# Optimization experiments

Measured on AMD Instinct MI355X. Metric: run time of the kernel, lower is better.

Reference implementation:

```python
import jax, jax.numpy as jnp
import numpy as np
import math

DIM = 512
HEADS = 8
DIM_HEAD = 64
INNER = HEADS * DIM_HEAD
B = 2
N = 2048


def _alibi_slopes(heads):
    def pow2(n):
        start = 2 ** (-2 ** (-(math.log2(n) - 3)))
        return [start * start ** i for i in range(n)]
    if math.log2(heads).is_integer():
        return pow2(heads)
    cp2 = 2 ** math.floor(math.log2(heads))
    return pow2(cp2) + pow2(2 * cp2)[0::2][: heads - cp2]


def setup_inputs() -> dict:
    key = jax.random.key(0)
    ks = jax.random.split(key, 9)
    s = 0.02
    return {
        "x": jax.random.normal(ks[0], (B, N, DIM), dtype=jnp.float32),
        "gamma": jnp.ones((DIM,), jnp.float32),
        "beta": jnp.zeros((DIM,), jnp.float32),
        "wq1": jax.random.normal(ks[1], (INNER, DIM), jnp.float32) * s,
        "wqd": jax.random.normal(ks[2], (INNER, 3), jnp.float32) * s,
        "wk1": jax.random.normal(ks[3], (INNER, DIM), jnp.float32) * s,
        "wkd": jax.random.normal(ks[4], (INNER, 3), jnp.float32) * s,
        "wv1": jax.random.normal(ks[5], (INNER, DIM), jnp.float32) * s,
        "wvd": jax.random.normal(ks[6], (INNER, 3), jnp.float32) * s,
        "wout": jax.random.normal(ks[7], (DIM, INNER), jnp.float32) * s,
    }


def _proj(xp, w1, wd):
    # xp: [b, dim, n+2] (already left-padded by 2)
    y = jnp.einsum('ed,bdn->ben', w1, xp)  # pointwise conv (kernel 1, no bias)
    # depthwise causal conv, kernel 3: valid conv after left pad of 2
    y = (wd[None, :, 0:1] * y[..., :-2]
         + wd[None, :, 1:2] * y[..., 1:-1]
         + wd[None, :, 2:3] * y[..., 2:])
    return y  # [b, inner, n]


def _split_heads(y, b, n):
    # [b, (h d), n] -> [b, h, n, d]
    return y.reshape(b, HEADS, DIM_HEAD, n).transpose(0, 1, 3, 2)


def reference(x, gamma, beta, wq1, wqd, wk1, wkd, wv1, wvd, wout):
    b, n, d = x.shape
    scale = DIM_HEAD ** -0.5
    # LayerNorm over last dim
    mu = jnp.mean(x, axis=-1, keepdims=True)
    var = jnp.var(x, axis=-1, keepdims=True)
    xn = (x - mu) / jnp.sqrt(var + 1e-5) * gamma + beta
    # b n d -> b d n, left pad 2
    xp = jnp.pad(xn.transpose(0, 2, 1), ((0, 0), (0, 0), (2, 0)))
    q = _split_heads(_proj(xp, wq1, wqd), b, n) * scale
    k = _split_heads(_proj(xp, wk1, wkd), b, n)
    v = _split_heads(_proj(xp, wv1, wvd), b, n)
    sim = jnp.einsum('bhid,bhjd->bhij', q, k)
    # ALiBi bias
    slopes = jnp.asarray(_alibi_slopes(HEADS), dtype=sim.dtype)  # [h]
    idx = jnp.arange(n)
    bias = -jnp.abs(idx[None, :] - idx[:, None]).astype(sim.dtype)  # [n, n]
    sim = sim + bias[None, None] * slopes[None, :, None, None]
    # causal mask
    causal = jnp.triu(jnp.ones((n, n), bool), 1)
    sim = jnp.where(causal[None, None], -jnp.finfo(sim.dtype).max, sim)
    attn = jax.nn.softmax(sim, axis=-1)
    out = jnp.einsum('bhij,bhjd->bhid', attn, v)
    out = out.transpose(0, 2, 1, 3).reshape(b, n, INNER)
    return out @ wout.T
```

## Files before the change

### kernel.cpp

```cpp
#include <hip/hip_runtime.h>
#include <hip/hip_bf16.h>
#include <math.h>

#define BATCH 2
#define NSEQ 2048
#define DIM 512
#define HEADS 8
#define DH 64
#define NTOK (BATCH * NSEQ)
#define NPROJ (3 * DIM)

typedef short short8 __attribute__((ext_vector_type(8)));
typedef short short4v __attribute__((ext_vector_type(4)));
typedef float f32x4 __attribute__((ext_vector_type(4)));
typedef float f32x16 __attribute__((ext_vector_type(16)));
typedef __hip_bfloat16 bf16;

static __device__ __forceinline__ short f2b(float f) {
    __hip_bfloat16 h = __float2bfloat16(f);
    return *(short*)&h;
}

static __device__ __forceinline__ void gload_lds16(const void* g, void* l) {
    __builtin_amdgcn_global_load_lds(
        (const __attribute__((address_space(1))) unsigned int*)g,
        (__attribute__((address_space(3))) unsigned int*)l, 16, 0, 0);
}

__global__ __launch_bounds__(128) void ln_kernel(
    const float* __restrict__ x, const float* __restrict__ gamma,
    const float* __restrict__ beta, bf16* __restrict__ xnb)
{
    int row = blockIdx.x;
    int tid = threadIdx.x;
    float4 v = ((const float4*)(x + (size_t)row * DIM))[tid];
    float s  = v.x + v.y + v.z + v.w;
    float s2 = v.x*v.x + v.y*v.y + v.z*v.z + v.w*v.w;
    #pragma unroll
    for (int off = 32; off > 0; off >>= 1) {
        s  += __shfl_down(s,  off);
        s2 += __shfl_down(s2, off);
    }
    __shared__ float red[4];
    if ((tid & 63) == 0) { red[(tid >> 6) * 2] = s; red[(tid >> 6) * 2 + 1] = s2; }
    __syncthreads();
    float S  = red[0] + red[2];
    float S2 = red[1] + red[3];
    float mu  = S * (1.0f / DIM);
    float var = S2 * (1.0f / DIM) - mu * mu;
    float inv = rsqrtf(var + 1e-5f);
    float4 g  = ((const float4*)gamma)[tid];
    float4 be = ((const float4*)beta)[tid];
    short4v o;
    o[0] = f2b((v.x - mu) * inv * g.x + be.x);
    o[1] = f2b((v.y - mu) * inv * g.y + be.y);
    o[2] = f2b((v.z - mu) * inv * g.z + be.z);
    o[3] = f2b((v.w - mu) * inv * g.w + be.w);
    ((short4v*)(xnb + (size_t)row * DIM))[tid] = o;
}

__global__ __launch_bounds__(256) void convert_w(
    const float* __restrict__ wq1, const float* __restrict__ wk1,
    const float* __restrict__ wv1, const float* __restrict__ wout,
    bf16* __restrict__ Wcat, bf16* __restrict__ woutb)
{
    int i4 = blockIdx.x * 256 + threadIdx.x;
    int base = i4 * 4;
    int which = base >> 18;
    int e = base & 262143;
    const float* src = which == 0 ? wq1 : which == 1 ? wk1 : which == 2 ? wv1 : wout;
    float4 v = *(const float4*)(src + e);
    bf16* dst = (which < 3) ? (Wcat + ((size_t)which << 18) + e) : (woutb + e);
    short4v o;
    o[0] = f2b(v.x); o[1] = f2b(v.y); o[2] = f2b(v.z); o[3] = f2b(v.w);
    *(short4v*)dst = o;
}

__global__ __launch_bounds__(256) void gemm_bf16_nt(
    const bf16* __restrict__ A, const bf16* __restrict__ W,
    float* __restrict__ C, int N, int K)
{
    __shared__ bf16 As[128 * 64];
    __shared__ bf16 Bs[128 * 64];
    int tid = threadIdx.x;
    int m0 = blockIdx.y * 128, n0 = blockIdx.x * 128;
    int lane = tid & 63;
    int w = tid >> 6;
    int wm = (w >> 1) * 64, wn = (w & 1) * 64;
    int l15 = lane & 15, l4 = lane >> 4;
    f32x4 acc[4][4] = {};
    for (int k0 = 0; k0 < K; k0 += 64) {
        __syncthreads();
        #pragma unroll
        for (int it = 0; it < 4; it++) {
            int s = it * 256 + tid;
            int row = s >> 3, cs = s & 7;
            gload_lds16(A + (size_t)(m0 + row) * K + k0 + cs * 8, As + s * 8);
            gload_lds16(W + (size_t)(n0 + row) * K + k0 + cs * 8, Bs + s * 8);
        }
        __syncthreads();
        #pragma unroll
        for (int kk = 0; kk < 64; kk += 32) {
            short8 af[4], bfr[4];
            #pragma unroll
            for (int m = 0; m < 4; m++)
                af[m] = *(const short8*)(As + (wm + m * 16 + l15) * 64 + kk + l4 * 8);
            #pragma unroll
            for (int n = 0; n < 4; n++)
                bfr[n] = *(const short8*)(Bs + (wn + n * 16 + l15) * 64 + kk + l4 * 8);
            #pragma unroll
            for (int m = 0; m < 4; m++)
                #pragma unroll
                for (int n = 0; n < 4; n++)
                    acc[m][n] = __builtin_amdgcn_mfma_f32_16x16x32_bf16(
                        af[m], bfr[n], acc[m][n], 0, 0, 0);
        }
    }
    #pragma unroll
    for (int m = 0; m < 4; m++)
        #pragma unroll
        for (int n = 0; n < 4; n++) {
            int row = m0 + wm + m * 16 + l4 * 4;
            int col = n0 + wn + n * 16 + l15;
            #pragma unroll
            for (int r = 0; r < 4; r++)
                C[(size_t)(row + r) * N + col] = acc[m][n][r];
        }
}

__global__ __launch_bounds__(256) void dwconv_kernel(
    const float* __restrict__ ycat,
    const float* __restrict__ wqd, const float* __restrict__ wkd, const float* __restrict__ wvd,
    bf16* __restrict__ q, bf16* __restrict__ k, bf16* __restrict__ v)
{
    int which = blockIdx.z;
    const float* wd = which == 0 ? wqd : which == 1 ? wkd : wvd;
    bf16* dst       = which == 0 ? q   : which == 1 ? k   : v;
    float scale     = which == 0 ? 0.125f : 1.0f;
    int idx = blockIdx.x * 256 + threadIdx.x;
    int e = idx & (DIM - 1);
    int t = idx >> 9;
    int n = t & (NSEQ - 1);
    const float* y = ycat + which * DIM;
    float y0 = y[(size_t)t * NPROJ + e];
    float y1 = (n >= 1) ? y[(size_t)(t - 1) * NPROJ + e] : 0.0f;
    float y2 = (n >= 2) ? y[(size_t)(t - 2) * NPROJ + e] : 0.0f;
    float w0 = wd[e * 3 + 0], w1 = wd[e * 3 + 1], w2 = wd[e * 3 + 2];
    float r = (w0 * y2 + w1 * y1 + w2 * y0) * scale;
    int b = t >> 11;
    int h = e >> 6, d = e & 63;
    dst[(((size_t)(b * HEADS + h)) * NSEQ + n) * DH + d] = __float2bfloat16(r);
}

__global__ __launch_bounds__(256) void vtrans_kernel(
    const bf16* __restrict__ v, bf16* __restrict__ vT)
{
    __shared__ unsigned short L[64][72];
    int bh = blockIdx.y;
    int n0 = blockIdx.x * 64;
    int tid = threadIdx.x;
    const unsigned short* src = (const unsigned short*)v + ((size_t)bh * NSEQ + n0) * DH;
    #pragma unroll
    for (int it = 0; it < 2; it++) {
        int idx = it * 256 + tid;
        int r = idx >> 3, c = (idx & 7) * 8;
        *(short8*)&L[r][c] = *(const short8*)(src + (size_t)r * DH + c);
    }
    __syncthreads();
    unsigned short* dst = (unsigned short*)vT + (size_t)bh * DH * NSEQ + n0;
    #pragma unroll
    for (int it = 0; it < 2; it++) {
        int idx = it * 256 + tid;
        int d = idx >> 3, c8 = (idx & 7) * 8;
        short8 o;
        #pragma unroll
        for (int t = 0; t < 8; t++) o[t] = (short)L[c8 + t][d];
        *(short8*)(dst + (size_t)d * NSEQ + c8) = o;
    }
}

struct KV { short8 kf[4]; short8 v0[2]; short8 v1[2]; };

__device__ __forceinline__ KV load_kv(
    const bf16* __restrict__ Kb, const unsigned short* __restrict__ vt,
    int j0, int il, int hi)
{
    KV r;
    const short8* krow = (const short8*)(Kb + (size_t)(j0 + il) * DH);
    #pragma unroll
    for (int c = 0; c < 4; c++) r.kf[c] = krow[2 * c + hi];
    #pragma unroll
    for (int jc = 0; jc < 2; jc++) {
        r.v0[jc] = *(const short8*)(vt + (size_t)il * NSEQ + j0 + jc * 16 + hi * 8);
        r.v1[jc] = *(const short8*)(vt + (size_t)(32 + il) * NSEQ + j0 + jc * 16 + hi * 8);
    }
    return r;
}

template<bool MASKED>
__device__ __forceinline__ void attn_step(
    const KV& kv, int j0, int il, int hi, int i_global,
    const short8* qf, const float* bconst, float slope2,
    f32x16& o0, f32x16& o1, float& lsum)
{
    f32x16 st = {};
    #pragma unroll
    for (int c = 0; c < 4; c++)
        st = __builtin_amdgcn_mfma_f32_32x32x16_bf16(kv.kf[c], qf[c], st, 0, 0, 0);
    float sdb = slope2 * (float)(j0 - i_global);
    float p[16];
    #pragma unroll
    for (int r = 0; r < 16; r++) {
        float e = fmaf(st[r], 1.4426950408889634f, sdb + bconst[r]);
        float pr = exp2f(e);
        if (MASKED) {
            int jl = (r & 3) + 8 * (r >> 2) + 4 * hi;
            pr = (jl <= il) ? pr : 0.0f;
        }
        p[r] = pr;
        lsum += pr;
    }
    unsigned w[8];
    #pragma unroll
    for (int g = 0; g < 4; g++) {
        asm("v_cvt_pk_bf16_f32 %0, %1, %2" : "=v"(w[2*g])   : "v"(p[4*g]),   "v"(p[4*g+1]));
        asm("v_cvt_pk_bf16_f32 %0, %1, %2" : "=v"(w[2*g+1]) : "v"(p[4*g+2]), "v"(p[4*g+3]));
    }
    #pragma unroll
    for (int jc = 0; jc < 2; jc++) {
        unsigned x0 = w[4*jc], x1 = w[4*jc+1], y0 = w[4*jc+2], y1 = w[4*jc+3];
        asm("v_permlane32_swap_b32 %0, %1" : "+v"(x0), "+v"(y0));
        asm("v_permlane32_swap_b32 %0, %1" : "+v"(x1), "+v"(y1));
        union { unsigned u[4]; short8 s; } pa;
        pa.u[0] = x0; pa.u[1] = x1; pa.u[2] = y0; pa.u[3] = y1;
        o0 = __builtin_amdgcn_mfma_f32_32x32x16_bf16(pa.s, kv.v0[jc], o0, 0, 0, 0);
        o1 = __builtin_amdgcn_mfma_f32_32x32x16_bf16(pa.s, kv.v1[jc], o1, 0, 0, 0);
    }
}

__global__ __launch_bounds__(64) void attn_mfma(
    const bf16* __restrict__ Q, const bf16* __restrict__ K,
    const bf16* __restrict__ VT, float* __restrict__ po, float* __restrict__ pl)
{
    int bh = blockIdx.y;
    int sp = blockIdx.z;
    int h = bh & (HEADS - 1);
    int ti = (blockIdx.x + 13 * blockIdx.y) & 63;
    int i0 = ti * 32;
    int lane = threadIdx.x;
    int il = lane & 31, hi = lane >> 5;
    int i_global = i0 + il;
    float slope2 = exp2f(-(float)(h + 1)) * 1.4426950408889634f;
    float bconst[16];
    #pragma unroll
    for (int r = 0; r < 16; r++) {
        int jl = (r & 3) + 8 * (r >> 2) + 4 * hi;
        bconst[r] = slope2 * (float)jl;
    }
    const bf16* Qb = Q + (size_t)bh * NSEQ * DH;
    const bf16* Kb = K + (size_t)bh * NSEQ * DH;
    const unsigned short* vt = (const unsigned short*)(VT + (size_t)bh * DH * NSEQ);
    short8 qf[4];
    const short8* qrow = (const short8*)(Qb + (size_t)(i0 + il) * DH);
    #pragma unroll
    for (int c = 0; c < 4; c++) qf[c] = qrow[2 * c + hi];
    f32x16 o0 = {}, o1 = {};
    float lsum = 0.0f;
    if (sp <= ti) {
        KV cur = load_kv(Kb, vt, sp * 32, il, hi);
        for (int kt = sp; kt <= ti; kt += 4) {
            KV nxt;
            bool more = (kt + 4) <= ti;
            if (more) nxt = load_kv(Kb, vt, (kt + 4) * 32, il, hi);
            if (kt == ti)
                attn_step<true >(cur, kt * 32, il, hi, i_global, qf, bconst, slope2, o0, o1, lsum);
            else
                attn_step<false>(cur, kt * 32, il, hi, i_global, qf, bconst, slope2, o0, o1, lsum);
            if (more) cur = nxt;
        }
    }
    float ltot = lsum + __shfl_xor(lsum, 32);
    size_t pbase = ((size_t)sp * (BATCH * HEADS) + bh) * NSEQ + i0;
    if (hi == 0) pl[pbase + il] = ltot;
    float* pop = po + pbase * DH;
    #pragma unroll
    for (int r = 0; r < 16; r++) {
        int irow = (r & 3) + 8 * (r >> 2) + 4 * hi;
        pop[(size_t)irow * DH + il]      = o0[r];
        pop[(size_t)irow * DH + 32 + il] = o1[r];
    }
}

__global__ __launch_bounds__(256) void merge_kernel(
    const float* __restrict__ pl, const float* __restrict__ po,
    bf16* __restrict__ attnb)
{
    int idx = blockIdx.x * 256 + threadIdx.x;
    int d = idx & 63;
    int rbh = idx >> 6;
    int n  = rbh & (NSEQ - 1);
    int bh = rbh >> 11;
    const size_t S = (size_t)(BATCH * HEADS) * NSEQ;
    float l = 0.0f, o = 0.0f;
    #pragma unroll
    for (int s = 0; s < 4; s++) {
        l += pl[(size_t)s * S + rbh];
        o += po[((size_t)s * S + rbh) * DH + d];
    }
    int b = bh >> 3, h = bh & 7;
    attnb[((size_t)(b * NSEQ + n)) * DIM + h * DH + d] = __float2bfloat16(o / l);
}

extern "C" void kernel_launch(void* const* d_in, const int* in_sizes, int n_in,
                              void* d_out, int out_size, void* d_ws, size_t ws_size,
                              hipStream_t stream)
{
    (void)in_sizes; (void)n_in; (void)out_size; (void)ws_size;
    const float* x     = (const float*)d_in[0];
    const float* gamma = (const float*)d_in[1];
    const float* beta  = (const float*)d_in[2];
    const float* wq1   = (const float*)d_in[3];
    const float* wqd   = (const float*)d_in[4];
    const float* wk1   = (const float*)d_in[5];
    const float* wkd   = (const float*)d_in[6];
    const float* wv1   = (const float*)d_in[7];
    const float* wvd   = (const float*)d_in[8];
    const float* wout  = (const float*)d_in[9];
    float* out = (float*)d_out;
    char* base = (char*)d_ws;

    const size_t MB = 1 << 20;
    bf16*  xnb   = (bf16*)(base);
    bf16*  Wcat  = (bf16*)(base + 4 * MB);
    bf16*  woutb = (bf16*)(base + 6 * MB);
    bf16*  qb    = (bf16*)(base + 7 * MB);
    bf16*  kb    = (bf16*)(base + 11 * MB);
    bf16*  vb    = (bf16*)(base + 15 * MB);
    bf16*  vtb   = (bf16*)(base + 19 * MB);
    bf16*  attnb = (bf16*)(base + 23 * MB);
    float* pl    = (float*)(base + 27 * MB);
    float* ycat  = (float*)(base + 32 * MB);
    float* po    = (float*)(base + 32 * MB);

    ln_kernel<<<NTOK, 128, 0, stream>>>(x, gamma, beta, xnb);
    convert_w<<<1024, 256, 0, stream>>>(wq1, wk1, wv1, wout, Wcat, woutb);
    gemm_bf16_nt<<<dim3(NPROJ / 128, NTOK / 128), 256, 0, stream>>>(
        xnb, Wcat, ycat, NPROJ, DIM);
    dwconv_kernel<<<dim3(NTOK * DIM / 256, 1, 3), 256, 0, stream>>>(
        ycat, wqd, wkd, wvd, qb, kb, vb);
    vtrans_kernel<<<dim3(NSEQ / 64, BATCH * HEADS), 256, 0, stream>>>(vb, vtb);
    attn_mfma<<<dim3(64, BATCH * HEADS, 4), 64, 0, stream>>>(qb, kb, vtb, po, pl);
    merge_kernel<<<(BATCH * HEADS * NSEQ * DH) / 256, 256, 0, stream>>>(pl, po, attnb);
    gemm_bf16_nt<<<dim3(DIM / 128, NTOK / 128), 256, 0, stream>>>(
        attnb, woutb, out, DIM, DIM);
}
```

Before: 180.1 us.

## Process two query tiles per attention block and vectorize dwconv and merge

The attention kernel now gives each wave two adjacent 32-row query tiles. Each K/V tile it loads is reused for both query tiles, halving K/V global traffic per query row. The kernel also reverses block order so the heaviest causal tiles launch first, and splits the K and V loads so only K is prefetched one step ahead. The depthwise-conv and merge kernels switch to float4 loads and 4-wide bf16 stores, and merge computes one reciprocal per row instead of dividing per element. In exchange there are half as many attention blocks and each uses more registers, which may reduce occupancy and parallelism.

```diff
diff --git a/kernel.cpp b/kernel.cpp
--- a/kernel.cpp
+++ b/kernel.cpp
@@ -138,18 +138,25 @@
     bf16* dst       = which == 0 ? q   : which == 1 ? k   : v;
     float scale     = which == 0 ? 0.125f : 1.0f;
     int idx = blockIdx.x * 256 + threadIdx.x;
-    int e = idx & (DIM - 1);
-    int t = idx >> 9;
-    int n = t & (NSEQ - 1);
-    const float* y = ycat + which * DIM;
-    float y0 = y[(size_t)t * NPROJ + e];
-    float y1 = (n >= 1) ? y[(size_t)(t - 1) * NPROJ + e] : 0.0f;
-    float y2 = (n >= 2) ? y[(size_t)(t - 2) * NPROJ + e] : 0.0f;
-    float w0 = wd[e * 3 + 0], w1 = wd[e * 3 + 1], w2 = wd[e * 3 + 2];
-    float r = (w0 * y2 + w1 * y1 + w2 * y0) * scale;
+    int e4 = idx & 127;
+    int t  = idx >> 7;
+    int n  = t & (NSEQ - 1);
+    int e  = e4 * 4;
+    const float* y = ycat + (size_t)t * NPROJ + which * DIM + e;
+    float4 zero = make_float4(0, 0, 0, 0);
+    float4 y0 = *(const float4*)y;
+    float4 y1 = (n >= 1) ? *(const float4*)(y - NPROJ) : zero;
+    float4 y2 = (n >= 2) ? *(const float4*)(y - 2 * NPROJ) : zero;
+    const float4* wp = (const float4*)(wd + e * 3);
+    float4 wA = wp[0], wB = wp[1], wC = wp[2];
+    short4v o;
+    o[0] = f2b((wA.x * y2.x + wA.y * y1.x + wA.z * y0.x) * scale);
+    o[1] = f2b((wA.w * y2.y + wB.x * y1.y + wB.y * y0.y) * scale);
+    o[2] = f2b((wB.z * y2.z + wB.w * y1.z + wC.x * y0.z) * scale);
+    o[3] = f2b((wC.y * y2.w + wC.z * y1.w + wC.w * y0.w) * scale);
     int b = t >> 11;
     int h = e >> 6, d = e & 63;
-    dst[(((size_t)(b * HEADS + h)) * NSEQ + n) * DH + d] = __float2bfloat16(r);
+    *(short4v*)(dst + (((size_t)(b * HEADS + h)) * NSEQ + n) * DH + d) = o;
 }
 
 __global__ __launch_bounds__(256) void vtrans_kernel(
@@ -179,16 +186,19 @@
     }
 }
 
-struct KV { short8 kf[4]; short8 v0[2]; short8 v1[2]; };
-
-__device__ __forceinline__ KV load_kv(
-    const bf16* __restrict__ Kb, const unsigned short* __restrict__ vt,
-    int j0, int il, int hi)
-{
-    KV r;
+struct Kf { short8 k[4]; };
+struct Vf { short8 v0[2]; short8 v1[2]; };
+
+__device__ __forceinline__ Kf load_k(const bf16* __restrict__ Kb, int j0, int il, int hi) {
+    Kf r;
     const short8* krow = (const short8*)(Kb + (size_t)(j0 + il) * DH);
     #pragma unroll
-    for (int c = 0; c < 4; c++) r.kf[c] = krow[2 * c + hi];
+    for (int c = 0; c < 4; c++) r.k[c] = krow[2 * c + hi];
+    return r;
+}
+
+__device__ __forceinline__ Vf load_v(const unsigned short* __restrict__ vt, int j0, int il, int hi) {
+    Vf r;
     #pragma unroll
     for (int jc = 0; jc < 2; jc++) {
         r.v0[jc] = *(const short8*)(vt + (size_t)il * NSEQ + j0 + jc * 16 + hi * 8);
@@ -198,15 +208,16 @@
 }
 
 template<bool MASKED>
-__device__ __forceinline__ void attn_step(
-    const KV& kv, int j0, int il, int hi, int i_global,
-    const short8* qf, const float* bconst, float slope2,
+__device__ __forceinline__ void tile_step(
+    const Kf& kf, const Vf& vf, const short8* qf,
+    int j0, int il, int hi, int i_global,
+    const float* bconst, float slope2,
     f32x16& o0, f32x16& o1, float& lsum)
 {
     f32x16 st = {};
     #pragma unroll
     for (int c = 0; c < 4; c++)
-        st = __builtin_amdgcn_mfma_f32_32x32x16_bf16(kv.kf[c], qf[c], st, 0, 0, 0);
+        st = __builtin_amdgcn_mfma_f32_32x32x16_bf16(kf.k[c], qf[c], st, 0, 0, 0);
     float sdb = slope2 * (float)(j0 - i_global);
     float p[16];
     #pragma unroll
@@ -233,52 +244,16 @@
         asm("v_permlane32_swap_b32 %0, %1" : "+v"(x1), "+v"(y1));
         union { unsigned u[4]; short8 s; } pa;
         pa.u[0] = x0; pa.u[1] = x1; pa.u[2] = y0; pa.u[3] = y1;
-        o0 = __builtin_amdgcn_mfma_f32_32x32x16_bf16(pa.s, kv.v0[jc], o0, 0, 0, 0);
-        o1 = __builtin_amdgcn_mfma_f32_32x32x16_bf16(pa.s, kv.v1[jc], o1, 0, 0, 0);
-    }
-}
-
-__global__ __launch_bounds__(64) void attn_mfma(
-    const bf16* __restrict__ Q, const bf16* __restrict__ K,
-    const bf16* __restrict__ VT, float* __restrict__ po, float* __restrict__ pl)
-{
-    int bh = blockIdx.y;
-    int sp = blockIdx.z;
-    int h = bh & (HEADS - 1);
-    int ti = (blockIdx.x + 13 * blockIdx.y) & 63;
-    int i0 = ti * 32;
-    int lane = threadIdx.x;
-    int il = lane & 31, hi = lane >> 5;
-    int i_global = i0 + il;
-    float slope2 = exp2f(-(float)(h + 1)) * 1.4426950408889634f;
-    float bconst[16];
-    #pragma unroll
-    for (int r = 0; r < 16; r++) {
-        int jl = (r & 3) + 8 * (r >> 2) + 4 * hi;
-        bconst[r] = slope2 * (float)jl;
-    }
-    const bf16* Qb = Q + (size_t)bh * NSEQ * DH;
-    const bf16* Kb = K + (size_t)bh * NSEQ * DH;
-    const unsigned short* vt = (const unsigned short*)(VT + (size_t)bh * DH * NSEQ);
-    short8 qf[4];
-    const short8* qrow = (const short8*)(Qb + (size_t)(i0 + il) * DH);
-    #pragma unroll
-    for (int c = 0; c < 4; c++) qf[c] = qrow[2 * c + hi];
-    f32x16 o0 = {}, o1 = {};
-    float lsum = 0.0f;
-    if (sp <= ti) {
-        KV cur = load_kv(Kb, vt, sp * 32, il, hi);
-        for (int kt = sp; kt <= ti; kt += 4) {
-            KV nxt;
-            bool more = (kt + 4) <= ti;
-            if (more) nxt = load_kv(Kb, vt, (kt + 4) * 32, il, hi);
-            if (kt == ti)
-                attn_step<true >(cur, kt * 32, il, hi, i_global, qf, bconst, slope2, o0, o1, lsum);
-            else
-                attn_step<false>(cur, kt * 32, il, hi, i_global, qf, bconst, slope2, o0, o1, lsum);
-            if (more) cur = nxt;
-        }
-    }
+        o0 = __builtin_amdgcn_mfma_f32_32x32x16_bf16(pa.s, vf.v0[jc], o0, 0, 0, 0);
+        o1 = __builtin_amdgcn_mfma_f32_32x32x16_bf16(pa.s, vf.v1[jc], o1, 0, 0, 0);
+    }
+}
+
+__device__ __forceinline__ void write_tile(
+    float* __restrict__ po, float* __restrict__ pl,
+    int sp, int bh, int i0, int il, int hi,
+    const f32x16& o0, const f32x16& o1, float lsum)
+{
     float ltot = lsum + __shfl_xor(lsum, 32);
     size_t pbase = ((size_t)sp * (BATCH * HEADS) + bh) * NSEQ + i0;
     if (hi == 0) pl[pbase + il] = ltot;
@@ -291,24 +266,83 @@
     }
 }
 
+__global__ __launch_bounds__(64) void attn_mfma(
+    const bf16* __restrict__ Q, const bf16* __restrict__ K,
+    const bf16* __restrict__ VT, float* __restrict__ po, float* __restrict__ pl)
+{
+    int t  = 31 - blockIdx.x;
+    int bh = blockIdx.y;
+    int sp = blockIdx.z;
+    int h = bh & (HEADS - 1);
+    int tiA = 2 * t, tiB = 2 * t + 1;
+    int i0A = tiA * 32, i0B = i0A + 32;
+    int lane = threadIdx.x;
+    int il = lane & 31, hi = lane >> 5;
+    float slope2 = exp2f(-(float)(h + 1)) * 1.4426950408889634f;
+    float bconst[16];
+    #pragma unroll
+    for (int r = 0; r < 16; r++) {
+        int jl = (r & 3) + 8 * (r >> 2) + 4 * hi;
+        bconst[r] = slope2 * (float)jl;
+    }
+    const bf16* Qb = Q + (size_t)bh * NSEQ * DH;
+    const bf16* Kb = K + (size_t)bh * NSEQ * DH;
+    const unsigned short* vt = (const unsigned short*)(VT + (size_t)bh * DH * NSEQ);
+    short8 qfA[4], qfB[4];
+    {
+        const short8* qra = (const short8*)(Qb + (size_t)(i0A + il) * DH);
+        const short8* qrb = (const short8*)(Qb + (size_t)(i0B + il) * DH);
+        #pragma unroll
+        for (int c = 0; c < 4; c++) { qfA[c] = qra[2 * c + hi]; qfB[c] = qrb[2 * c + hi]; }
+    }
+    f32x16 oA0 = {}, oA1 = {}, oB0 = {}, oB1 = {};
+    float lsA = 0.0f, lsB = 0.0f;
+
+    Kf kcur = load_k(Kb, sp * 32, il, hi);
+    for (int kt = sp; kt <= tiB; kt += 4) {
+        int j0 = kt * 32;
+        Vf vf = load_v(vt, j0, il, hi);
+        int jn = (kt + 4 <= tiB) ? (kt + 4) * 32 : j0;
+        Kf knxt = load_k(Kb, jn, il, hi);
+        if (kt < tiA) {
+            tile_step<false>(kcur, vf, qfA, j0, il, hi, i0A + il, bconst, slope2, oA0, oA1, lsA);
+            tile_step<false>(kcur, vf, qfB, j0, il, hi, i0B + il, bconst, slope2, oB0, oB1, lsB);
+        } else if (kt == tiA) {
+            tile_step<true >(kcur, vf, qfA, j0, il, hi, i0A + il, bconst, slope2, oA0, oA1, lsA);
+            tile_step<false>(kcur, vf, qfB, j0, il, hi, i0B + il, bconst, slope2, oB0, oB1, lsB);
+        } else {
+            tile_step<true >(kcur, vf, qfB, j0, il, hi, i0B + il, bconst, slope2, oB0, oB1, lsB);
+        }
+        kcur = knxt;
+    }
+    write_tile(po, pl, sp, bh, i0A, il, hi, oA0, oA1, lsA);
+    write_tile(po, pl, sp, bh, i0B, il, hi, oB0, oB1, lsB);
+}
+
 __global__ __launch_bounds__(256) void merge_kernel(
     const float* __restrict__ pl, const float* __restrict__ po,
     bf16* __restrict__ attnb)
 {
     int idx = blockIdx.x * 256 + threadIdx.x;
-    int d = idx & 63;
-    int rbh = idx >> 6;
+    int d = (idx & 15) * 4;
+    int rbh = idx >> 4;
     int n  = rbh & (NSEQ - 1);
     int bh = rbh >> 11;
     const size_t S = (size_t)(BATCH * HEADS) * NSEQ;
-    float l = 0.0f, o = 0.0f;
+    float l = 0.0f;
+    float ox = 0, oy = 0, oz = 0, ow = 0;
     #pragma unroll
     for (int s = 0; s < 4; s++) {
         l += pl[(size_t)s * S + rbh];
-        o += po[((size_t)s * S + rbh) * DH + d];
-    }
+        float4 p = *(const float4*)(po + ((size_t)s * S + rbh) * DH + d);
+        ox += p.x; oy += p.y; oz += p.z; ow += p.w;
+    }
+    float inv = 1.0f / l;
     int b = bh >> 3, h = bh & 7;
-    attnb[((size_t)(b * NSEQ + n)) * DIM + h * DH + d] = __float2bfloat16(o / l);
+    short4v o;
+    o[0] = f2b(ox * inv); o[1] = f2b(oy * inv);
+    o[2] = f2b(oz * inv); o[3] = f2b(ow * inv);
+    *(short4v*)(attnb + ((size_t)(b * NSEQ + n)) * DIM + h * DH + d) = o;
 }
 
 extern "C" void kernel_launch(void* const* d_in, const int* in_sizes, int n_in,
@@ -346,11 +380,11 @@
     convert_w<<<1024, 256, 0, stream>>>(wq1, wk1, wv1, wout, Wcat, woutb);
     gemm_bf16_nt<<<dim3(NPROJ / 128, NTOK / 128), 256, 0, stream>>>(
         xnb, Wcat, ycat, NPROJ, DIM);
-    dwconv_kernel<<<dim3(NTOK * DIM / 256, 1, 3), 256, 0, stream>>>(
+    dwconv_kernel<<<dim3(NTOK * 128 / 256, 1, 3), 256, 0, stream>>>(
         ycat, wqd, wkd, wvd, qb, kb, vb);
     vtrans_kernel<<<dim3(NSEQ / 64, BATCH * HEADS), 256, 0, stream>>>(vb, vtb);
-    attn_mfma<<<dim3(64, BATCH * HEADS, 4), 64, 0, stream>>>(qb, kb, vtb, po, pl);
-    merge_kernel<<<(BATCH * HEADS * NSEQ * DH) / 256, 256, 0, stream>>>(pl, po, attnb);
+    attn_mfma<<<dim3(32, BATCH * HEADS, 4), 64, 0, stream>>>(qb, kb, vtb, po, pl);
+    merge_kernel<<<(BATCH * HEADS * NSEQ * 16) / 256, 256, 0, stream>>>(pl, po, attnb);
     gemm_bf16_nt<<<dim3(DIM / 128, NTOK / 128), 256, 0, stream>>>(
         attnb, woutb, out, DIM, DIM);
 }
```

Result: no change. 179.0 us (-0.6%).
